# Kernel optimization log

Measured on AMD Instinct MI355X. Metric: run time of the kernel, lower is better.

## Reference

```python
import jax, jax.numpy as jnp
import numpy as np

MUL = 16          # env_embed_multiplicity
LAT = 128         # latent dim
NUM_LAYERS = 2
AVG_N = 20.0      # avg_num_neighbors -> env_sum_normalizations = rsqrt(avg_n)
P = 6.0           # PolynomialCutoff_p


def _mlp(x, w1, w2):
    # ScalarMLPFunction: Linear -> SiLU -> Linear
    return jax.nn.silu(x @ w1) @ w2


def _poly_cutoff(u, p=P):
    f = (1.0 - ((p + 1.0) * (p + 2.0) / 2.0) * u ** p
         + p * (p + 2.0) * u ** (p + 1.0)
         - (p * (p + 1.0) / 2.0) * u ** (p + 2.0))
    return jnp.where(u < 1.0, f, 0.0)


def _weighter(attr, w):
    # MakeWeightedChannels: attr [E,4] = 1x0e + 1x1o, w [E, MUL*2] (one weight per irrep per channel)
    w = w.reshape(-1, MUL, 2)
    fs = w[:, :, 0] * attr[:, 0:1]                    # [E,MUL] scalar channel
    fv = w[:, :, 1][:, :, None] * attr[:, None, 1:4]  # [E,MUL,3] vector channel
    return fs, fv


def _forward(edge_attr, node_attrs, edge_embed, edge_u,
             w2b1, w2b2, lat1_w1, lat1_w2, env0_w1, env0_w2, env1_w1, env1_w2,
             l2w0_w1, l2w0_w2, l2w1_w1, l2w1_w2, envlin_ws, envlin_wv,
             fl2w_w1, fl2w_w2, edge_index):
    E = edge_attr.shape[0]
    N = node_attrs.shape[0]
    center, neigh = edge_index[0], edge_index[1]
    cut = _poly_cutoff(edge_u)[:, None]               # per-layer cutoffs all = r_max
    norm = np.float32(1.0 / np.sqrt(AVG_N))
    inv_s3 = np.float32(1.0 / np.sqrt(3.0))           # CG norm for 1x1->0
    inv_s2 = np.float32(1.0 / np.sqrt(2.0))           # CG norm for 1x1->1 (cross)
    inv_sm = np.float32(1.0 / np.sqrt(MUL))

    # two-body latent: cat(center types, neighbor types, radial embedding)
    x2b = jnp.concatenate([node_attrs[center], node_attrs[neigh], edge_embed], axis=-1)
    lat = cut * _mlp(x2b, w2b1, w2b2)                 # [E,LAT]
    w0 = _mlp(lat, env0_w1, env0_w2)                  # [E,4*MUL] = edge-embed + env weights
    w_edge, w_env = w0[:, :2 * MUL], w0[:, 2 * MUL:]
    fs, fv = _weighter(edge_attr, w_edge)             # initial edge features (embed_initial_edge)

    latent_in = None
    for l in range(NUM_LAYERS):
        if l > 0:
            # latent resnet (update param = 0 -> sigmoid(0))
            new_lat = cut * _mlp(latent_in, lat1_w1, lat1_w2)
            a = np.float32(jax.nn.sigmoid(0.0))
            c_old = np.float32(1.0 / np.sqrt(a * a + 1.0))
            lat = c_old * lat + (a * c_old) * new_lat
            w_env = _mlp(lat, env1_w1, env1_w2)
        # weighted environment embedding: scatter-sum over neighbors, normalize
        es_e, ev_e = _weighter(edge_attr, w_env)
        env_s = jax.ops.segment_sum(es_e, center, num_segments=N) * norm   # [N,MUL]
        env_v = jax.ops.segment_sum(ev_e, center, num_segments=N) * norm   # [N,MUL,3]
        # env_linear (per-irrep channel mixing)
        env_s = (env_s @ envlin_ws[l]) * inv_sm
        env_v = jnp.einsum('nui,uv->nvi', env_v, envlin_wv[l]) * inv_sm
        es, ev = env_s[center], env_v[center]          # gather back to edges
        # channelwise ('uuu') tensor product, lmax=1: 2 scalar + 3 vector paths
        s1 = fs * es
        s2 = jnp.sum(fv * ev, axis=-1) * inv_s3
        v1 = fs[:, :, None] * ev
        v2 = fv * es[:, :, None]
        v3 = jnp.cross(fv, ev) * inv_s2
        scalars = jnp.stack([s1, s2], axis=-1).reshape(E, 2 * MUL)
        latent_in = jnp.concatenate([lat, scalars], axis=-1)      # [E, LAT+2*MUL]
        # per-edge generated linear (shared_weights=False)
        lw1, lw2 = (l2w0_w1, l2w0_w2) if l == 0 else (l2w1_w1, l2w1_w2)
        lw = _mlp(latent_in, lw1, lw2)                 # [E, 5*MUL*MUL]
        ws = lw[:, :2 * MUL * MUL].reshape(E, 2, MUL, MUL)
        wv = lw[:, 2 * MUL * MUL:].reshape(E, 3, MUL, MUL)
        S = jnp.stack([s1, s2], axis=1)                # [E,2,MUL]
        V = jnp.stack([v1, v2, v3], axis=1)            # [E,3,MUL,3]
        fs = jnp.einsum('epu,epuv->ev', S, ws) * np.float32(1.0 / np.sqrt(2.0 * MUL))
        fv = jnp.einsum('epui,epuv->evi', V, wv) * np.float32(1.0 / np.sqrt(3.0 * MUL))
    # final per-edge linear -> 1x1o output per edge
    fw = _mlp(latent_in, fl2w_w1, fl2w_w2)             # [E,MUL]
    return jnp.einsum('eu,eui->ei', fw, fv) * inv_sm   # [E,3]


def setup_inputs():
    key = jax.random.key(0)
    ks = jax.random.split(key, 24)
    E, N, T, B = 120000, 5000, 4, 8
    def w(k, i, o):
        return jax.random.normal(k, (i, o), jnp.float32) / np.float32(np.sqrt(i))
    return {
        'edge_attr': jax.random.normal(ks[0], (E, 4), jnp.float32),
        'node_attrs': jax.random.uniform(ks[1], (N, T), jnp.float32),
        'edge_embed': jax.random.uniform(ks[2], (E, B), jnp.float32),
        'edge_u': jax.random.uniform(ks[3], (E,), jnp.float32),
        'edge_index': jax.random.randint(ks[4], (2, E), 0, N, jnp.int32),
        'w2b1': w(ks[5], 2 * T + B, LAT), 'w2b2': w(ks[6], LAT, LAT),
        'lat1_w1': w(ks[7], LAT + 2 * MUL, LAT), 'lat1_w2': w(ks[8], LAT, LAT),
        'env0_w1': w(ks[9], LAT, LAT), 'env0_w2': w(ks[10], LAT, 4 * MUL),
        'env1_w1': w(ks[11], LAT, LAT), 'env1_w2': w(ks[12], LAT, 2 * MUL),
        'l2w0_w1': w(ks[13], LAT + 2 * MUL, LAT), 'l2w0_w2': w(ks[14], LAT, 5 * MUL * MUL),
        'l2w1_w1': w(ks[15], LAT + 2 * MUL, LAT), 'l2w1_w2': w(ks[16], LAT, 5 * MUL * MUL),
        'envlin_ws': jax.random.normal(ks[17], (NUM_LAYERS, MUL, MUL), jnp.float32),
        'envlin_wv': jax.random.normal(ks[18], (NUM_LAYERS, MUL, MUL), jnp.float32),
        'fl2w_w1': w(ks[19], LAT + 2 * MUL, LAT), 'fl2w_w2': w(ks[20], LAT, MUL),
    }


def reference(edge_attr, node_attrs, edge_embed, edge_u, edge_index,
              w2b1, w2b2, lat1_w1, lat1_w2, env0_w1, env0_w2, env1_w1, env1_w2,
              l2w0_w1, l2w0_w2, l2w1_w1, l2w1_w2, envlin_ws, envlin_wv,
              fl2w_w1, fl2w_w2):
    return _forward(edge_attr, node_attrs, edge_embed, edge_u,
                    w2b1, w2b2, lat1_w1, lat1_w2, env0_w1, env0_w2, env1_w1, env1_w2,
                    l2w0_w1, l2w0_w2, l2w1_w1, l2w1_w2, envlin_ws, envlin_wv,
                    fl2w_w1, fl2w_w2, edge_index)
```

## Files before the change

kernel.cpp:

```cpp
#include <hip/hip_runtime.h>

typedef _Float16 half_t;
typedef _Float16 half8 __attribute__((ext_vector_type(8)));
typedef _Float16 half2_t __attribute__((ext_vector_type(2)));
typedef float f32x16 __attribute__((ext_vector_type(16)));
typedef float f32x4 __attribute__((ext_vector_type(4)));

#define DEVINL __device__ __forceinline__

#define INV_S3 0.57735026918962576f
#define INV_S2 0.70710678118654752f
#define C_OLD  0.89442719099991588f
#define A_COLD 0.44721359549995794f
#define SC_ENV 0.05590169943749474f
#define SC_FS  0.17677669529663688f
#define SC_FV  0.14433756729740643f
#define SC_OUT 0.03608439182435161f
#define SSD 34
#define VPH 146

DEVINL float silu_f(float x) { return x / (1.f + __expf(-x)); }

DEVINL float poly_cut(float u) {
    float u2 = u * u, u4 = u2 * u2, u6 = u4 * u2;
    float f = 1.f - 28.f * u6 + 48.f * u6 * u - 21.f * u6 * u2;
    return (u < 1.f) ? f : 0.f;
}

DEVINL float pkh(float a, float b) {
    half2_t h; h[0] = (half_t)a; h[1] = (half_t)b;
    return __builtin_bit_cast(float, h);
}
DEVINL float2 uph(float p) {
    half2_t h = __builtin_bit_cast(half2_t, p);
    return make_float2((float)h[0], (float)h[1]);
}
DEVINL half8 mk8(const float* w) {
    f32x4 v = {w[0], w[1], w[2], w[3]};
    return __builtin_bit_cast(half8, v);
}
DEVINL float ld_pk2(const half_t* p) {
    half2_t h; h[0] = p[0]; h[1] = p[1];
    return __builtin_bit_cast(float, h);
}
DEVINL float ntl_f(const float* p) { return __builtin_nontemporal_load(p); }
DEVINL f32x4 ntl_f4(const void* p) {
    return __builtin_nontemporal_load((const f32x4*)p);
}
DEVINL f32x4 ld_f4(const void* p) { return *reinterpret_cast<const f32x4*>(p); }
DEVINL void st_h8(half8 v, half_t* p) { *reinterpret_cast<half8*>(p) = v; }
DEVINL void st_f4(const f32x4& v, float* p) { *reinterpret_cast<f32x4*>(p) = v; }

template <int KB>
DEVINL f32x16 colstage(const half_t* __restrict__ Wg, const float* B, int mtile,
                       int nl, int q) {
    const half_t* ap = Wg + (((size_t)mtile * KB + q) * 32 + nl) * 8;
    constexpr int H = KB / 2;
    f32x16 acc0;
#pragma unroll
    for (int i = 0; i < 16; ++i) acc0[i] = 0.f;
    if constexpr (H < 2) {
        half8 a = *reinterpret_cast<const half8*>(ap);
        acc0 = __builtin_amdgcn_mfma_f32_32x32x16_f16(a, mk8(B), acc0, 0, 0, 0);
        return acc0;
    } else {
        f32x16 acc1;
#pragma unroll
        for (int i = 0; i < 16; ++i) acc1[i] = 0.f;
#pragma unroll
        for (int h = 0; h + 1 < H; h += 2) {
            half8 a0 = *reinterpret_cast<const half8*>(ap + h * 512);
            half8 a1 = *reinterpret_cast<const half8*>(ap + (h + 1) * 512);
            acc0 = __builtin_amdgcn_mfma_f32_32x32x16_f16(a0, mk8(B + h * 4), acc0, 0, 0, 0);
            acc1 = __builtin_amdgcn_mfma_f32_32x32x16_f16(a1, mk8(B + (h + 1) * 4), acc1, 0, 0, 0);
        }
        if constexpr (H & 1) {
            half8 a = *reinterpret_cast<const half8*>(ap + (H - 1) * 512);
            acc0 = __builtin_amdgcn_mfma_f32_32x32x16_f16(a, mk8(B + (H - 1) * 4), acc0, 0, 0, 0);
        }
        return acc0 + acc1;
    }
}

template <int KB>
DEVINL f32x16 colstage_lds(const half_t* W, const float* B, int nl, int q) {
    const half_t* ap = W + (q * 32 + nl) * 8;
    constexpr int H = KB / 2;
    f32x16 acc0, acc1;
#pragma unroll
    for (int i = 0; i < 16; ++i) { acc0[i] = 0.f; acc1[i] = 0.f; }
#pragma unroll
    for (int h = 0; h + 1 < H; h += 2) {
        half8 a0 = *reinterpret_cast<const half8*>(ap + h * 512);
        half8 a1 = *reinterpret_cast<const half8*>(ap + (h + 1) * 512);
        acc0 = __builtin_amdgcn_mfma_f32_32x32x16_f16(a0, mk8(B + h * 4), acc0, 0, 0, 0);
        acc1 = __builtin_amdgcn_mfma_f32_32x32x16_f16(a1, mk8(B + (h + 1) * 4), acc1, 0, 0, 0);
    }
    if constexpr (H & 1) {
        half8 a = *reinterpret_cast<const half8*>(ap + (H - 1) * 512);
        acc0 = __builtin_amdgcn_mfma_f32_32x32x16_f16(a, mk8(B + (H - 1) * 4), acc0, 0, 0, 0);
    }
    return acc0 + acc1;
}

struct WFrag { half8 a[8]; };

DEVINL f32x16 mfma8w(const WFrag& f, const float* B) {
    f32x16 acc0, acc1;
#pragma unroll
    for (int i = 0; i < 16; ++i) { acc0[i] = 0.f; acc1[i] = 0.f; }
#pragma unroll
    for (int h = 0; h < 8; h += 2) {
        acc0 = __builtin_amdgcn_mfma_f32_32x32x16_f16(f.a[h], mk8(B + h * 4), acc0, 0, 0, 0);
        acc1 = __builtin_amdgcn_mfma_f32_32x32x16_f16(f.a[h + 1], mk8(B + (h + 1) * 4), acc1, 0, 0, 0);
    }
    return acc0 + acc1;
}

DEVINL void silu16(f32x16& a) {
#pragma unroll
    for (int i = 0; i < 16; ++i) a[i] = silu_f(a[i]);
}

DEVINL void d2b(const f32x16& d, int lane, int q, float* wA, float* wB) {
    float pk[8];
#pragma unroll
    for (int a2 = 0; a2 < 4; ++a2) {
        pk[a2 * 2 + 0] = pkh(d[4 * a2 + 0], d[4 * a2 + 1]);
        pk[a2 * 2 + 1] = pkh(d[4 * a2 + 2], d[4 * a2 + 3]);
    }
#pragma unroll
    for (int t = 0; t < 2; ++t) {
        float k0 = q ? pk[(2 * t + 1) * 2 + 0] : pk[(2 * t) * 2 + 0];
        float k1 = q ? pk[(2 * t + 1) * 2 + 1] : pk[(2 * t) * 2 + 1];
        float s0 = q ? pk[(2 * t) * 2 + 0] : pk[(2 * t + 1) * 2 + 0];
        float s1 = q ? pk[(2 * t) * 2 + 1] : pk[(2 * t + 1) * 2 + 1];
        float r0 = __shfl(s0, lane ^ 32, 64);
        float r1 = __shfl(s1, lane ^ 32, 64);
        float* w = t ? wB : wA;
        w[0] = q ? r0 : k0;
        w[1] = q ? r1 : k1;
        w[2] = q ? k0 : r0;
        w[3] = q ? k1 : r1;
    }
}

DEVINL void ld5(const f32x4* src, f32x4* st, int tid) {
#pragma unroll
    for (int k = 0; k < 5; ++k) st[k] = ld_f4(src + k * 128 + tid);
}
DEVINL void ld4(const f32x4* src, f32x4* st, int tid) {
#pragma unroll
    for (int k = 0; k < 4; ++k) st[k] = ld_f4(src + k * 128 + tid);
}
DEVINL void wr5(f32x4* dst, const f32x4* st, int tid) {
#pragma unroll
    for (int k = 0; k < 5; ++k) dst[k * 128 + tid] = st[k];
}
DEVINL void wr4(f32x4* dst, const f32x4* st, int tid) {
#pragma unroll
    for (int k = 0; k < 4; ++k) dst[k * 128 + tid] = st[k];
}

__global__ __launch_bounds__(256) void k_zero(float* __restrict__ p, int n) {
    int i = blockIdx.x * 256 + threadIdx.x;
    if (i < n) p[i] = 0.f;
}

struct PackArgs {
    const float* src[14];
    half_t* dst[14];
    int K[14];
    int N[14];
};

__global__ __launch_bounds__(256) void k_pack(PackArgs pa) {
    int mi = blockIdx.y;
    int K = pa.K[mi], N = pa.N[mi];
    int Npad = (N + 31) & ~31;
    int KB = K >> 3;
    int cells = KB * Npad;
    int cell = blockIdx.x * 256 + threadIdx.x;
    if (cell >= cells) return;
    int nn = cell & 31, r2 = cell >> 5;
    int kblk = r2 % KB, ntile = r2 / KB;
    int n = ntile * 32 + nn;
    const float* W = pa.src[mi];
    half8 v;
#pragma unroll
    for (int j = 0; j < 8; ++j) {
        int k = kblk * 8 + j;
        v[j] = (half_t)((n < N) ? W[k * N + n] : 0.f);
    }
    *reinterpret_cast<half8*>(pa.dst[mi] + (size_t)cell * 8) = v;
}

__global__ __launch_bounds__(256) void k_hist(const int* __restrict__ eidx,
                                              int* __restrict__ cnt, int E) {
    int e = blockIdx.x * 256 + threadIdx.x;
    if (e < E) atomicAdd(&cnt[eidx[e]], 1);
}

__global__ __launch_bounds__(1024) void k_scan(const int* __restrict__ cnt,
                                               int* __restrict__ start,
                                               int* __restrict__ cursor, int Nn) {
    __shared__ int sh[1024];
    const int t = threadIdx.x;
    const int C = 5;
    int base = t * C;
    int local[C];
    int s = 0;
#pragma unroll
    for (int j = 0; j < C; ++j) {
        int idx = base + j;
        int v = (idx < Nn) ? cnt[idx] : 0;
        local[j] = v;
        s += v;
    }
    sh[t] = s;
    __syncthreads();
    for (int off = 1; off < 1024; off <<= 1) {
        int v = (t >= off) ? sh[t - off] : 0;
        __syncthreads();
        sh[t] += v;
        __syncthreads();
    }
    int run = sh[t] - s;
#pragma unroll
    for (int j = 0; j < C; ++j) {
        int idx = base + j;
        if (idx < Nn) {
            start[idx] = run;
            cursor[idx] = run;
            run += local[j];
        }
    }
    if (t == 1023) start[Nn] = sh[1023];
}

__global__ __launch_bounds__(256) void k_bucket(const int* __restrict__ eidx,
                                                int* __restrict__ cursor,
                                                int* __restrict__ eord, int E) {
    int e = blockIdx.x * 256 + threadIdx.x;
    if (e < E) {
        int pos = atomicAdd(&cursor[eidx[e]], 1);
        eord[pos] = e;
    }
}

__global__ __launch_bounds__(128, 4) void k_edge_front(
    const float* __restrict__ g_ea, const float* __restrict__ g_na,
    const float* __restrict__ g_emb, const float* __restrict__ g_eu,
    const int* __restrict__ g_eidx,
    const half_t* __restrict__ b_w2b1, const half_t* __restrict__ b_w2b2,
    const half_t* __restrict__ b_e0w1, const half_t* __restrict__ b_e0w2,
    half_t* __restrict__ g_lat0, float* __restrict__ g_fs, float* __restrict__ g_fv,
    float* __restrict__ contrib, int E) {
    const int lane = threadIdx.x & 63, nl = lane & 31, q = lane >> 5;
    const int g = blockIdx.x * 2 + (threadIdx.x >> 6);
    const int e = g * 32 + nl;
    int ce = g_eidx[e];
    (void)ce;
    float4 ea = *reinterpret_cast<const float4*>(g_ea + e * 4);
    float cut = poly_cut(g_eu[e]);

    float xw[4];
    if (q == 0) {
        int ce0 = g_eidx[e];
        int ne = g_eidx[E + e];
        float4 nc = *reinterpret_cast<const float4*>(g_na + ce0 * 4);
        float4 nn = *reinterpret_cast<const float4*>(g_na + ne * 4);
        xw[0] = pkh(nc.x, nc.y); xw[1] = pkh(nc.z, nc.w);
        xw[2] = pkh(nn.x, nn.y); xw[3] = pkh(nn.z, nn.w);
    } else {
        f32x4 m0 = ntl_f4(g_emb + e * 8);
        f32x4 m1 = ntl_f4(g_emb + e * 8 + 4);
        xw[0] = pkh(m0[0], m0[1]); xw[1] = pkh(m0[2], m0[3]);
        xw[2] = pkh(m1[0], m1[1]); xw[3] = pkh(m1[2], m1[3]);
    }

    float hB[32], lB[32];
#pragma unroll
    for (int c = 0; c < 4; ++c) {
        f32x16 d = colstage<2>(b_w2b1, xw, c, nl, q);
        silu16(d);
        d2b(d, lane, q, &hB[8 * c], &hB[8 * c + 4]);
    }
    half_t* gl = g_lat0 + (size_t)g * 4096;
#pragma unroll
    for (int c = 0; c < 4; ++c) {
        f32x16 d = colstage<16>(b_w2b2, hB, c, nl, q);
#pragma unroll
        for (int i = 0; i < 16; ++i) d[i] *= cut;
        d2b(d, lane, q, &lB[8 * c], &lB[8 * c + 4]);
        st_h8(mk8(&lB[8 * c]), gl + ((4 * c + q) * 32 + nl) * 8);
        st_h8(mk8(&lB[8 * c + 4]), gl + ((4 * c + 2 + q) * 32 + nl) * 8);
    }
#pragma unroll
    for (int c = 0; c < 4; ++c) {
        f32x16 d = colstage<16>(b_e0w1, lB, c, nl, q);
        silu16(d);
        d2b(d, lane, q, &hB[8 * c], &hB[8 * c + 4]);
    }
    {
        f32x16 d0 = colstage<16>(b_e0w2, hB, 0, nl, q);
        f32x16 d1 = colstage<16>(b_e0w2, hB, 1, nl, q);
        float* cp = contrib + (size_t)e * 64;
#pragma unroll
        for (int r = 0; r < 16; ++r) {
            int f = (r & 3) + 8 * (r >> 2) + 4 * q;
            int u = f >> 1;
            float v0 = d0[r], v1 = d1[r];
            if ((f & 1) == 0) {
                g_fs[e * 16 + u] = v0 * ea.x;
                cp[u] = v1 * ea.x;
            } else {
                g_fv[e * 48 + u * 3 + 0] = v0 * ea.y;
                g_fv[e * 48 + u * 3 + 1] = v0 * ea.z;
                g_fv[e * 48 + u * 3 + 2] = v0 * ea.w;
                cp[16 + u * 3 + 0] = v1 * ea.y;
                cp[16 + u * 3 + 1] = v1 * ea.z;
                cp[16 + u * 3 + 2] = v1 * ea.w;
            }
        }
    }
}

__global__ __launch_bounds__(256) void k_node_agg(
    const int* __restrict__ start, const int* __restrict__ eord,
    const float* __restrict__ contrib, const float* __restrict__ wls,
    const float* __restrict__ wlv, float* __restrict__ ls,
    float* __restrict__ lv, int Nn) {
    __shared__ float rawsh[4][64];
    const int t = threadIdx.x & 63;
    const int sub = threadIdx.x >> 6;
    const int n = blockIdx.x * 4 + sub;
    float acc = 0.f;
    if (n < Nn) {
        int s = start[n], en = start[n + 1];
        for (int base = s; base < en; base += 64) {
            int m = en - base; if (m > 64) m = 64;
            int myord = (base + t < en) ? eord[base + t] : 0;
            for (int i = 0; i < m; ++i) {
                int e2 = __shfl(myord, i, 64);
                acc += contrib[(size_t)e2 * 64 + t];
            }
        }
    }
    rawsh[sub][t] = acc;
    __syncthreads();
    if (n < Nn) {
        const float* raws = rawsh[sub];
        if (t < 16) {
            float as = 0.f;
#pragma unroll
            for (int u = 0; u < 16; ++u) as = fmaf(raws[u], wls[u * 16 + t], as);
            ls[n * 16 + t] = as * SC_ENV;
        } else {
            int idx = t - 16;
            int v = idx / 3, c = idx - 3 * v;
            float a = 0.f;
#pragma unroll
            for (int u = 0; u < 16; ++u)
                a = fmaf(raws[16 + u * 3 + c], wlv[u * 16 + v], a);
            lv[n * 48 + v * 3 + c] = a * SC_ENV;
        }
    }
}

__global__ __launch_bounds__(128, 2) void k_foldlat(
    const float* __restrict__ g_ea, const float* __restrict__ g_eu,
    const int* __restrict__ g_eidx,
    const float* __restrict__ g_fs, const float* __restrict__ g_fv,
    float* __restrict__ gfs2, float* __restrict__ gfv2,
    const float* __restrict__ ls0, const float* __restrict__ lv0,
    const half_t* __restrict__ b_lat1w1, const half_t* __restrict__ b_lat1w2,
    const half_t* __restrict__ b_e1w1, const half_t* __restrict__ b_e1w2,
    const half_t* __restrict__ b_gw1, const half_t* __restrict__ b_gw2,
    const half_t* __restrict__ g_lat0, half_t* __restrict__ g_lat1,
    float* __restrict__ contrib, int nblk2, int E) {
    __shared__ __align__(16) char smem[39424];
    const int tid = threadIdx.x;
    const int lane = tid & 63, nl = lane & 31, q = lane >> 5;
    const int wid = tid >> 6;
    const int bid = blockIdx.x;

    if (bid < nblk2) {
        half_t* sS = reinterpret_cast<half_t*>(smem) + wid * (32 * SSD);
        half_t* Vsh = reinterpret_cast<half_t*>(smem + 4352) + wid * (32 * VPH);
        f32x4* Wb0 = reinterpret_cast<f32x4*>(smem + 23040);
        f32x4* Wb1 = Wb0 + 512;
        const int g = bid * 2 + wid;
        const int e = g * 32 + nl;
        int ce = g_eidx[e];

        const f32x4* gsrc = reinterpret_cast<const f32x4*>(b_gw2);
        f32x4 st[4];
#pragma unroll
        for (int k = 0; k < 4; ++k) st[k] = ld_f4(gsrc + k * 128 + tid);

#pragma unroll
        for (int mm = 0; mm < 8; ++mm) {
            int m = q * 8 + mm;
            float fs = ntl_f(g_fs + e * 16 + m);
            float fv0 = ntl_f(g_fv + e * 48 + m * 3 + 0);
            float fv1 = ntl_f(g_fv + e * 48 + m * 3 + 1);
            float fv2 = ntl_f(g_fv + e * 48 + m * 3 + 2);
            float es = ls0[ce * 16 + m];
            float ev0 = lv0[ce * 48 + m * 3 + 0];
            float ev1 = lv0[ce * 48 + m * 3 + 1];
            float ev2 = lv0[ce * 48 + m * 3 + 2];
            sS[nl * SSD + 2 * m + 0] = (half_t)(fs * es);
            sS[nl * SSD + 2 * m + 1] =
                (half_t)((fv0 * ev0 + fv1 * ev1 + fv2 * ev2) * INV_S3);
            half_t* vp = Vsh + nl * VPH;
            vp[m * 3 + 0] = (half_t)(fs * ev0);
            vp[m * 3 + 1] = (half_t)(fs * ev1);
            vp[m * 3 + 2] = (half_t)(fs * ev2);
            vp[(16 + m) * 3 + 0] = (half_t)(fv0 * es);
            vp[(16 + m) * 3 + 1] = (half_t)(fv1 * es);
            vp[(16 + m) * 3 + 2] = (half_t)(fv2 * es);
            vp[(32 + m) * 3 + 0] = (half_t)((fv1 * ev2 - fv2 * ev1) * INV_S2);
            vp[(32 + m) * 3 + 1] = (half_t)((fv2 * ev0 - fv0 * ev2) * INV_S2);
            vp[(32 + m) * 3 + 2] = (half_t)((fv0 * ev1 - fv1 * ev0) * INV_S2);
        }

        float lB[40];
        const half_t* gl0 = g_lat0 + (size_t)g * 4096;
#pragma unroll
        for (int h = 0; h < 8; ++h) {
            f32x4 v = ntl_f4(gl0 + ((2 * h + q) * 32 + nl) * 8);
            lB[h * 4 + 0] = v[0]; lB[h * 4 + 1] = v[1];
            lB[h * 4 + 2] = v[2]; lB[h * 4 + 3] = v[3];
        }
        __syncthreads();

#pragma unroll
        for (int j2 = 0; j2 < 4; ++j2) {
            lB[32 + j2] = ld_pk2(sS + nl * SSD + 8 * q + 2 * j2);
            lB[36 + j2] = ld_pk2(sS + nl * SSD + 16 + 8 * q + 2 * j2);
        }

        float hB[32];
#pragma unroll
        for (int c = 0; c < 4; ++c) {
            f32x16 d = colstage<20>(b_gw1, lB, c, nl, q);
            silu16(d);
            d2b(d, lane, q, &hB[8 * c], &hB[8 * c + 4]);
        }

#pragma unroll
        for (int k = 0; k < 4; ++k) Wb0[k * 128 + tid] = st[k];
        __syncthreads();

        float fsacc[8];
        float fvacc[8][3];
#pragma unroll
        for (int s = 0; s < 8; ++s) {
            fsacc[s] = 0.f;
            fvacc[s][0] = fvacc[s][1] = fvacc[s][2] = 0.f;
        }

        for (int c = 0; c < 40; ++c) {
            const int buf = c & 1;
            f32x4* cur = buf ? Wb1 : Wb0;
            f32x4* nxt = buf ? Wb0 : Wb1;
            if (c + 1 < 40) {
#pragma unroll
                for (int k = 0; k < 4; ++k)
                    st[k] = ld_f4(gsrc + (size_t)(c + 1) * 512 + k * 128 + tid);
            }
            f32x16 d;
            {
                WFrag f;
                const half_t* wp = reinterpret_cast<const half_t*>(cur);
#pragma unroll
                for (int h = 0; h < 8; ++h)
                    f.a[h] = *reinterpret_cast<const half8*>(
                        wp + ((q + 2 * h) * 32 + nl) * 8);
                d = mfma8w(f, hB);
            }
            if (c < 16) {
                int pu0 = 2 * c, pu1 = pu0 + 1;
                float S0 = (float)sS[nl * SSD + 2 * (pu0 & 15) + (pu0 >> 4)];
                float S1 = (float)sS[nl * SSD + 2 * (pu1 & 15) + (pu1 >> 4)];
#pragma unroll
                for (int r = 0; r < 16; ++r) {
                    int a = r >> 2, bb = r & 3, slot = (a & 1) * 4 + bb;
                    fsacc[slot] = fmaf((a < 2) ? S0 : S1, d[r], fsacc[slot]);
                }
            } else {
                int w0i = 2 * c - 32, w1i = w0i + 1;
                const half_t* vp = Vsh + nl * VPH;
                float V00 = (float)vp[w0i * 3], V01 = (float)vp[w0i * 3 + 1], V02 = (float)vp[w0i * 3 + 2];
                float V10 = (float)vp[w1i * 3], V11 = (float)vp[w1i * 3 + 1], V12 = (float)vp[w1i * 3 + 2];
#pragma unroll
                for (int r = 0; r < 16; ++r) {
                    int a = r >> 2, bb = r & 3, slot = (a & 1) * 4 + bb;
                    float x0 = (a < 2) ? V00 : V10;
                    float x1 = (a < 2) ? V01 : V11;
                    float x2 = (a < 2) ? V02 : V12;
                    fvacc[slot][0] = fmaf(x0, d[r], fvacc[slot][0]);
                    fvacc[slot][1] = fmaf(x1, d[r], fvacc[slot][1]);
                    fvacc[slot][2] = fmaf(x2, d[r], fvacc[slot][2]);
                }
            }
            __builtin_amdgcn_sched_barrier(0);
            if (c + 1 < 40) {
#pragma unroll
                for (int k = 0; k < 4; ++k) nxt[k * 128 + tid] = st[k];
            }
            __syncthreads();
        }

        {
            float* fp = gfs2 + e * 16 + 4 * q;
            f32x4 flo = {fsacc[0] * SC_FS, fsacc[1] * SC_FS,
                         fsacc[2] * SC_FS, fsacc[3] * SC_FS};
            f32x4 fhi = {fsacc[4] * SC_FS, fsacc[5] * SC_FS,
                         fsacc[6] * SC_FS, fsacc[7] * SC_FS};
            st_f4(flo, fp);
            st_f4(fhi, fp + 8);
            float t2[24];
#pragma unroll
            for (int s = 0; s < 4; ++s) {
#pragma unroll
                for (int c3 = 0; c3 < 3; ++c3) {
                    t2[s * 3 + c3] = fvacc[s][c3] * SC_FV;
                    t2[12 + s * 3 + c3] = fvacc[4 + s][c3] * SC_FV;
                }
            }
            float* vlo = gfv2 + e * 48 + 12 * q;
            float* vhi = gfv2 + e * 48 + 24 + 12 * q;
#pragma unroll
            for (int i = 0; i < 3; ++i) {
                f32x4 a = {t2[4 * i + 0], t2[4 * i + 1], t2[4 * i + 2], t2[4 * i + 3]};
                f32x4 b = {t2[12 + 4 * i + 0], t2[12 + 4 * i + 1],
                           t2[12 + 4 * i + 2], t2[12 + 4 * i + 3]};
                st_f4(a, vlo + 4 * i);
                st_f4(b, vhi + 4 * i);
            }
        }
    } else {
        half_t* sS = reinterpret_cast<half_t*>(smem) + wid * (32 * SSD);
        f32x4* Wb0 = reinterpret_cast<f32x4*>(smem + 4352);
        f32x4* Wb1 = Wb0 + 640;
        const int b = bid - nblk2;
        const int g = b * 2 + wid;
        const int e = g * 32 + nl;
        int ce = g_eidx[e];

        const f32x4* w11 = reinterpret_cast<const f32x4*>(b_lat1w1);
        const f32x4* w12 = reinterpret_cast<const f32x4*>(b_lat1w2);
        const f32x4* w21 = reinterpret_cast<const f32x4*>(b_e1w1);
        const f32x4* w22 = reinterpret_cast<const f32x4*>(b_e1w2);

        f32x4 st[5];
        ld5(w11, st, tid);

#pragma unroll
        for (int mm = 0; mm < 8; ++mm) {
            int m = q * 8 + mm;
            float fs = ntl_f(g_fs + e * 16 + m);
            float fv0 = ntl_f(g_fv + e * 48 + m * 3 + 0);
            float fv1 = ntl_f(g_fv + e * 48 + m * 3 + 1);
            float fv2 = ntl_f(g_fv + e * 48 + m * 3 + 2);
            float es = ls0[ce * 16 + m];
            float ev0 = lv0[ce * 48 + m * 3 + 0];
            float ev1 = lv0[ce * 48 + m * 3 + 1];
            float ev2 = lv0[ce * 48 + m * 3 + 2];
            sS[nl * SSD + 2 * m + 0] = (half_t)(fs * es);
            sS[nl * SSD + 2 * m + 1] =
                (half_t)((fv0 * ev0 + fv1 * ev1 + fv2 * ev2) * INV_S3);
        }

        float lB[40];
        const half_t* gl0 = g_lat0 + (size_t)g * 4096;
#pragma unroll
        for (int h = 0; h < 8; ++h) {
            f32x4 v = ntl_f4(gl0 + ((2 * h + q) * 32 + nl) * 8);
            lB[h * 4 + 0] = v[0]; lB[h * 4 + 1] = v[1];
            lB[h * 4 + 2] = v[2]; lB[h * 4 + 3] = v[3];
        }
        float4 ea = *reinterpret_cast<const float4*>(g_ea + e * 4);
        float cut = poly_cut(g_eu[e]);

        wr5(Wb0, st, tid);
        __syncthreads();

#pragma unroll
        for (int j2 = 0; j2 < 4; ++j2) {
            lB[32 + j2] = ld_pk2(sS + nl * SSD + 8 * q + 2 * j2);
            lB[36 + j2] = ld_pk2(sS + nl * SSD + 16 + 8 * q + 2 * j2);
        }

        float hB[32];
#pragma unroll
        for (int c = 0; c < 4; ++c) {
            if (c < 3) ld5(w11 + (size_t)(c + 1) * 640, st, tid);
            else       ld4(w12, st, tid);
            f32x16 d = colstage_lds<20>(
                reinterpret_cast<const half_t*>((c & 1) ? Wb1 : Wb0), lB, nl, q);
            silu16(d);
            d2b(d, lane, q, &hB[8 * c], &hB[8 * c + 4]);
            __builtin_amdgcn_sched_barrier(0);
            if (c < 3) wr5(((c + 1) & 1) ? Wb1 : Wb0, st, tid);
            else       wr4(((c + 1) & 1) ? Wb1 : Wb0, st, tid);
            __syncthreads();
        }
        half_t* gl1 = g_lat1 + (size_t)g * 4096;
        float sc = A_COLD * cut;
#pragma unroll
        for (int c = 0; c < 4; ++c) {
            if (c < 3) ld4(w12 + (size_t)(c + 1) * 512, st, tid);
            else       ld4(w21, st, tid);
            f32x16 d = colstage_lds<16>(
                reinterpret_cast<const half_t*>((c & 1) ? Wb1 : Wb0), hB, nl, q);
#pragma unroll
            for (int i = 0; i < 16; ++i) d[i] *= sc;
            float nw[8];
            d2b(d, lane, q, nw, nw + 4);
#pragma unroll
            for (int p = 0; p < 8; ++p) {
                float2 o = uph(lB[8 * c + p]);
                float2 nn2 = uph(nw[p]);
                lB[8 * c + p] = pkh(C_OLD * o.x + nn2.x, C_OLD * o.y + nn2.y);
            }
            st_h8(mk8(&lB[8 * c]), gl1 + ((4 * c + q) * 32 + nl) * 8);
            st_h8(mk8(&lB[8 * c + 4]), gl1 + ((4 * c + 2 + q) * 32 + nl) * 8);
            __builtin_amdgcn_sched_barrier(0);
            wr4(((c + 1) & 1) ? Wb1 : Wb0, st, tid);
            __syncthreads();
        }
#pragma unroll
        for (int c = 0; c < 4; ++c) {
            if (c == 3) ld4(w22, st, tid);
            f32x16 d = colstage_lds<16>(
                reinterpret_cast<const half_t*>((c & 1) ? Wb1 : Wb0), lB, nl, q);
            silu16(d);
            d2b(d, lane, q, &hB[8 * c], &hB[8 * c + 4]);
            if (c < 3) ld4(w21 + (size_t)(c + 1) * 512, st, tid);
            __builtin_amdgcn_sched_barrier(0);
            wr4(((c + 1) & 1) ? Wb1 : Wb0, st, tid);
            __syncthreads();
        }
        {
            f32x16 d = colstage_lds<16>(
                reinterpret_cast<const half_t*>(Wb0), hB, nl, q);
            float* cp = contrib + (size_t)e * 64;
#pragma unroll
            for (int r = 0; r < 16; ++r) {
                int f = (r & 3) + 8 * (r >> 2) + 4 * q;
                int u = f >> 1;
                float val = d[r];
                if ((f & 1) == 0) {
                    cp[u] = val * ea.x;
                } else {
                    cp[16 + u * 3 + 0] = val * ea.y;
                    cp[16 + u * 3 + 1] = val * ea.z;
                    cp[16 + u * 3 + 2] = val * ea.w;
                }
            }
        }
    }
}

__global__ __launch_bounds__(128, 2) void k_layer1(
    const int* __restrict__ g_eidx, const float* __restrict__ gfs2,
    const float* __restrict__ gfv2, const float* __restrict__ ls1,
    const float* __restrict__ lv1,
    const half_t* __restrict__ b_flw1, const half_t* __restrict__ b_flw2,
    const half_t* __restrict__ b_gw1, const half_t* __restrict__ b_gw2,
    const half_t* __restrict__ g_lat1, float* __restrict__ g_out, int E) {
    __shared__ half_t sS2[2][32 * SSD];
    __shared__ half_t Vsh2[2][32 * VPH];
    __shared__ f32x4 Wbuf[2][640];
    const int tid = threadIdx.x;
    const int lane = tid & 63, nl = lane & 31, q = lane >> 5;
    const int wid = tid >> 6;
    const int g = blockIdx.x * 2 + wid;
    const int e = g * 32 + nl;
    int ce = g_eidx[e];
    half_t* sS = sS2[wid];
    half_t* Vsh = Vsh2[wid];

    const f32x4* wf1 = reinterpret_cast<const f32x4*>(b_flw1);
    const f32x4* wf2 = reinterpret_cast<const f32x4*>(b_flw2);
    const f32x4* wg1 = reinterpret_cast<const f32x4*>(b_gw1);
    const f32x4* wg2 = reinterpret_cast<const f32x4*>(b_gw2);

    f32x4 st[5];
    ld5(wf1, st, tid);

#pragma unroll
    for (int mm = 0; mm < 8; ++mm) {
        int m = q * 8 + mm;
        float fs = ntl_f(gfs2 + e * 16 + m);
        float fv0 = ntl_f(gfv2 + e * 48 + m * 3 + 0);
        float fv1 = ntl_f(gfv2 + e * 48 + m * 3 + 1);
        float fv2 = ntl_f(gfv2 + e * 48 + m * 3 + 2);
        float es = ls1[ce * 16 + m];
        float ev0 = lv1[ce * 48 + m * 3 + 0];
        float ev1 = lv1[ce * 48 + m * 3 + 1];
        float ev2 = lv1[ce * 48 + m * 3 + 2];
        sS[nl * SSD + 2 * m + 0] = (half_t)(fs * es);
        sS[nl * SSD + 2 * m + 1] =
            (half_t)((fv0 * ev0 + fv1 * ev1 + fv2 * ev2) * INV_S3);
        half_t* vp = Vsh + nl * VPH;
        vp[m * 3 + 0] = (half_t)(fs * ev0);
        vp[m * 3 + 1] = (half_t)(fs * ev1);
        vp[m * 3 + 2] = (half_t)(fs * ev2);
        vp[(16 + m) * 3 + 0] = (half_t)(fv0 * es);
        vp[(16 + m) * 3 + 1] = (half_t)(fv1 * es);
        vp[(16 + m) * 3 + 2] = (half_t)(fv2 * es);
        vp[(32 + m) * 3 + 0] = (half_t)((fv1 * ev2 - fv2 * ev1) * INV_S2);
        vp[(32 + m) * 3 + 1] = (half_t)((fv2 * ev0 - fv0 * ev2) * INV_S2);
        vp[(32 + m) * 3 + 2] = (half_t)((fv0 * ev1 - fv1 * ev0) * INV_S2);
    }

    float lB[40];
    const half_t* gl1 = g_lat1 + (size_t)g * 4096;
#pragma unroll
    for (int h = 0; h < 8; ++h) {
        f32x4 v = ntl_f4(gl1 + ((2 * h + q) * 32 + nl) * 8);
        lB[h * 4 + 0] = v[0]; lB[h * 4 + 1] = v[1];
        lB[h * 4 + 2] = v[2]; lB[h * 4 + 3] = v[3];
    }

    wr5(&Wbuf[0][0], st, tid);
    __syncthreads();

#pragma unroll
    for (int j2 = 0; j2 < 4; ++j2) {
        lB[32 + j2] = ld_pk2(sS + nl * SSD + 8 * q + 2 * j2);
        lB[36 + j2] = ld_pk2(sS + nl * SSD + 16 + 8 * q + 2 * j2);
    }

    float hB[32];
#pragma unroll
    for (int c = 0; c < 4; ++c) {
        if (c < 3) ld5(wf1 + (size_t)(c + 1) * 640, st, tid);
        else       ld4(wf2, st, tid);
        f32x16 d = colstage_lds<20>(
            reinterpret_cast<const half_t*>(&Wbuf[c & 1][0]), lB, nl, q);
        silu16(d);
        d2b(d, lane, q, &hB[8 * c], &hB[8 * c + 4]);
        __builtin_amdgcn_sched_barrier(0);
        if (c < 3) wr5(&Wbuf[(c + 1) & 1][0], st, tid);
        else       wr4(&Wbuf[(c + 1) & 1][0], st, tid);
        __syncthreads();
    }
    float fw[8];
    {
        ld5(wg1, st, tid);
        f32x16 d = colstage_lds<16>(
            reinterpret_cast<const half_t*>(&Wbuf[0][0]), hB, nl, q);
#pragma unroll
        for (int r = 0; r < 8; ++r) fw[r] = d[r];
        __builtin_amdgcn_sched_barrier(0);
        wr5(&Wbuf[1][0], st, tid);
        __syncthreads();
    }
#pragma unroll
    for (int c = 0; c < 4; ++c) {
        if (c < 3) ld5(wg1 + (size_t)(c + 1) * 640, st, tid);
        else       ld4(wg2 + (size_t)16 * 512, st, tid);
        f32x16 d = colstage_lds<20>(
            reinterpret_cast<const half_t*>(&Wbuf[(c + 1) & 1][0]), lB, nl, q);
        silu16(d);
        d2b(d, lane, q, &hB[8 * c], &hB[8 * c + 4]);
        __builtin_amdgcn_sched_barrier(0);
        if (c < 3) wr5(&Wbuf[c & 1][0], st, tid);
        else       wr4(&Wbuf[c & 1][0], st, tid);
        __syncthreads();
    }
    float fvacc[8][3];
#pragma unroll
    for (int s = 0; s < 8; ++s) fvacc[s][0] = fvacc[s][1] = fvacc[s][2] = 0.f;
    for (int j = 0; j < 24; ++j) {
        const int pb = (j + 1) & 1;
        if (j < 23) {
#pragma unroll
            for (int k = 0; k < 4; ++k)
                st[k] = ld_f4(wg2 + (size_t)(17 + j) * 512 + k * 128 + tid);
        }
        f32x16 d;
        {
            WFrag f;
            const half_t* wp = reinterpret_cast<const half_t*>(&Wbuf[pb][0]);
#pragma unroll
            for (int h = 0; h < 8; ++h)
                f.a[h] = *reinterpret_cast<const half8*>(
                    wp + ((q + 2 * h) * 32 + nl) * 8);
            d = mfma8w(f, hB);
        }
        {
            int w0i = 2 * j, w1i = 2 * j + 1;
            const half_t* vp = Vsh + nl * VPH;
            float V00 = (float)vp[w0i * 3], V01 = (float)vp[w0i * 3 + 1], V02 = (float)vp[w0i * 3 + 2];
            float V10 = (float)vp[w1i * 3], V11 = (float)vp[w1i * 3 + 1], V12 = (float)vp[w1i * 3 + 2];
#pragma unroll
            for (int r = 0; r < 16; ++r) {
                int a = r >> 2, bb = r & 3, slot = (a & 1) * 4 + bb;
                float x0 = (a < 2) ? V00 : V10;
                float x1 = (a < 2) ? V01 : V11;
                float x2 = (a < 2) ? V02 : V12;
                fvacc[slot][0] = fmaf(x0, d[r], fvacc[slot][0]);
                fvacc[slot][1] = fmaf(x1, d[r], fvacc[slot][1]);
                fvacc[slot][2] = fmaf(x2, d[r], fvacc[slot][2]);
            }
        }
        __builtin_amdgcn_sched_barrier(0);
        if (j < 23) wr4(&Wbuf[pb ^ 1][0], st, tid);
        __syncthreads();
    }
    {
        float o0 = 0.f, o1 = 0.f, o2 = 0.f;
#pragma unroll
        for (int s = 0; s < 8; ++s) {
            o0 = fmaf(fw[s], fvacc[s][0], o0);
            o1 = fmaf(fw[s], fvacc[s][1], o1);
            o2 = fmaf(fw[s], fvacc[s][2], o2);
        }
        o0 += __shfl(o0, lane ^ 32, 64);
        o1 += __shfl(o1, lane ^ 32, 64);
        o2 += __shfl(o2, lane ^ 32, 64);
        if (q == 0) {
            g_out[e * 3 + 0] = o0 * SC_OUT;
            g_out[e * 3 + 1] = o1 * SC_OUT;
            g_out[e * 3 + 2] = o2 * SC_OUT;
        }
    }
}

extern "C" void kernel_launch(void* const* d_in, const int* in_sizes, int n_in,
                              void* d_out, int out_size, void* d_ws, size_t ws_size,
                              hipStream_t stream) {
    const float* g_ea = (const float*)d_in[0];
    const float* g_na = (const float*)d_in[1];
    const float* g_emb = (const float*)d_in[2];
    const float* g_eu = (const float*)d_in[3];
    const int* g_eidx = (const int*)d_in[4];
    const float* w2b1 = (const float*)d_in[5];
    const float* w2b2 = (const float*)d_in[6];
    const float* lat1w1 = (const float*)d_in[7];
    const float* lat1w2 = (const float*)d_in[8];
    const float* e0w1 = (const float*)d_in[9];
    const float* e0w2 = (const float*)d_in[10];
    const float* e1w1 = (const float*)d_in[11];
    const float* e1w2 = (const float*)d_in[12];
    const float* l2w0w1 = (const float*)d_in[13];
    const float* l2w0w2 = (const float*)d_in[14];
    const float* l2w1w1 = (const float*)d_in[15];
    const float* l2w1w2 = (const float*)d_in[16];
    const float* envws = (const float*)d_in[17];
    const float* envwv = (const float*)d_in[18];
    const float* flw1 = (const float*)d_in[19];
    const float* flw2 = (const float*)d_in[20];
    float* out = (float*)d_out;

    const int E = in_sizes[3];
    const int Nn = in_sizes[1] / 4;
    const int nblk = E / 32;
    const int nblk2 = nblk / 2;

    float* p = (float*)d_ws;
    float* gfs = p;  p += (size_t)E * 16;
    float* gfv = p;  p += (size_t)E * 48;
    float* gfs2 = p; p += (size_t)E * 16;
    float* gfv2 = p; p += (size_t)E * 48;
    float* contrib = p; p += (size_t)E * 64;
    float* ls0 = p;  p += (size_t)Nn * 16;
    float* lv0 = p;  p += (size_t)Nn * 48;
    float* ls1 = p;  p += (size_t)Nn * 16;
    float* lv1 = p;  p += (size_t)Nn * 48;
    half_t* hp = (half_t*)p;
    half_t* lat0h = hp; hp += (size_t)nblk * 4096;
    half_t* lat1h = hp; hp += (size_t)nblk * 4096;

    const int KN[14][2] = {{16, 128}, {128, 128}, {128, 128}, {128, 64},
                           {160, 128}, {128, 128}, {128, 128}, {128, 32},
                           {160, 128}, {128, 1280}, {160, 128}, {128, 1280},
                           {160, 128}, {128, 16}};
    const float* srcs[14] = {w2b1, w2b2, e0w1, e0w2, lat1w1, lat1w2, e1w1, e1w2,
                             l2w0w1, l2w0w2, l2w1w1, l2w1w2, flw1, flw2};
    PackArgs pa;
    half_t* bptr[14];
    for (int i = 0; i < 14; ++i) {
        int K = KN[i][0], N = KN[i][1];
        int Npad = (N + 31) & ~31;
        bptr[i] = hp;
        hp += (size_t)K * Npad;
        pa.src[i] = srcs[i];
        pa.dst[i] = bptr[i];
        pa.K[i] = K;
        pa.N[i] = N;
    }
    int* ip = (int*)hp;
    int* cnt = ip;    ip += Nn;
    int* cursor = ip; ip += Nn;
    int* startp = ip; ip += Nn + 1;
    int* eord = ip;   ip += E;

    k_pack<<<dim3(80, 14), 256, 0, stream>>>(pa);
    k_zero<<<(Nn + 255) / 256, 256, 0, stream>>>((float*)cnt, Nn);
    k_hist<<<(E + 255) / 256, 256, 0, stream>>>(g_eidx, cnt, E);
    k_scan<<<1, 1024, 0, stream>>>(cnt, startp, cursor, Nn);
    k_bucket<<<(E + 255) / 256, 256, 0, stream>>>(g_eidx, cursor, eord, E);

    k_edge_front<<<nblk2, 128, 0, stream>>>(g_ea, g_na, g_emb, g_eu, g_eidx,
                                            bptr[0], bptr[1], bptr[2], bptr[3],
                                            lat0h, gfs, gfv, contrib, E);
    const int nagg = (Nn + 3) / 4;
    k_node_agg<<<nagg, 256, 0, stream>>>(startp, eord, contrib, envws, envwv,
                                         ls0, lv0, Nn);
    k_foldlat<<<nblk, 128, 0, stream>>>(g_ea, g_eu, g_eidx, gfs, gfv, gfs2, gfv2,
                                        ls0, lv0, bptr[4], bptr[5], bptr[6],
                                        bptr[7], bptr[8], bptr[9], lat0h, lat1h,
                                        contrib, nblk2, E);
    k_node_agg<<<nagg, 256, 0, stream>>>(startp, eord, contrib, envws + 256,
                                         envwv + 256, ls1, lv1, Nn);
    k_layer1<<<nblk2, 128, 0, stream>>>(g_eidx, gfs2, gfv2, ls1, lv1,
                                        bptr[12], bptr[13], bptr[10], bptr[11],
                                        lat1h, out, E);
}
```

Measured before the change: 436.4 us.

## Stage edge-front MLP weights through double-buffered LDS with prefetch

The edge-front kernel now stages each weight column block (w2b2, env0 w1, env0 w2) into a double-buffered shared-memory tile, prefetching the next block into registers while the current matmul stage reads from LDS. The aim is to replace repeated per-wave global weight loads with one cooperative load per block, overlapped with the MFMA work. It adds block-wide barriers and 16 KB of LDS per block, and it lowers the launch-bounds occupancy hint from 4 to 2 blocks.

```diff
diff --git a/kernel.cpp b/kernel.cpp
--- a/kernel.cpp
+++ b/kernel.cpp
@@ -248,7 +248,7 @@
     }
 }
 
-__global__ __launch_bounds__(128, 4) void k_edge_front(
+__global__ __launch_bounds__(128, 2) void k_edge_front(
     const float* __restrict__ g_ea, const float* __restrict__ g_na,
     const float* __restrict__ g_emb, const float* __restrict__ g_eu,
     const int* __restrict__ g_eidx,
@@ -256,13 +256,21 @@
     const half_t* __restrict__ b_e0w1, const half_t* __restrict__ b_e0w2,
     half_t* __restrict__ g_lat0, float* __restrict__ g_fs, float* __restrict__ g_fv,
     float* __restrict__ contrib, int E) {
-    const int lane = threadIdx.x & 63, nl = lane & 31, q = lane >> 5;
-    const int g = blockIdx.x * 2 + (threadIdx.x >> 6);
+    __shared__ f32x4 Wbuf[2][512];
+    const int tid = threadIdx.x;
+    const int lane = tid & 63, nl = lane & 31, q = lane >> 5;
+    const int wid = tid >> 6;
+    const int g = blockIdx.x * 2 + wid;
     const int e = g * 32 + nl;
-    int ce = g_eidx[e];
-    (void)ce;
     float4 ea = *reinterpret_cast<const float4*>(g_ea + e * 4);
     float cut = poly_cut(g_eu[e]);
+
+    const f32x4* s_w2b2 = reinterpret_cast<const f32x4*>(b_w2b2);
+    const f32x4* s_e0w1 = reinterpret_cast<const f32x4*>(b_e0w1);
+    const f32x4* s_e0w2 = reinterpret_cast<const f32x4*>(b_e0w2);
+
+    f32x4 st[4];
+    ld4(s_w2b2, st, tid);
 
     float xw[4];
     if (q == 0) {
@@ -286,25 +294,50 @@
         silu16(d);
         d2b(d, lane, q, &hB[8 * c], &hB[8 * c + 4]);
     }
+
+    wr4(&Wbuf[0][0], st, tid);
+    __syncthreads();
+
     half_t* gl = g_lat0 + (size_t)g * 4096;
 #pragma unroll
     for (int c = 0; c < 4; ++c) {
-        f32x16 d = colstage<16>(b_w2b2, hB, c, nl, q);
+        if (c < 3) ld4(s_w2b2 + (size_t)(c + 1) * 512, st, tid);
+        else       ld4(s_e0w1, st, tid);
+        f32x16 d = colstage_lds<16>(
+            reinterpret_cast<const half_t*>(&Wbuf[c & 1][0]), hB, nl, q);
 #pragma unroll
         for (int i = 0; i < 16; ++i) d[i] *= cut;
         d2b(d, lane, q, &lB[8 * c], &lB[8 * c + 4]);
         st_h8(mk8(&lB[8 * c]), gl + ((4 * c + q) * 32 + nl) * 8);
         st_h8(mk8(&lB[8 * c + 4]), gl + ((4 * c + 2 + q) * 32 + nl) * 8);
+        __builtin_amdgcn_sched_barrier(0);
+        wr4(&Wbuf[(c + 1) & 1][0], st, tid);
+        __syncthreads();
     }
 #pragma unroll
     for (int c = 0; c < 4; ++c) {
-        f32x16 d = colstage<16>(b_e0w1, lB, c, nl, q);
+        if (c < 3) ld4(s_e0w1 + (size_t)(c + 1) * 512, st, tid);
+        else       ld4(s_e0w2, st, tid);
+        f32x16 d = colstage_lds<16>(
+            reinterpret_cast<const half_t*>(&Wbuf[c & 1][0]), lB, nl, q);
         silu16(d);
         d2b(d, lane, q, &hB[8 * c], &hB[8 * c + 4]);
-    }
+        __builtin_amdgcn_sched_barrier(0);
+        wr4(&Wbuf[(c + 1) & 1][0], st, tid);
+        __syncthreads();
+    }
+    f32x16 d0, d1;
     {
-        f32x16 d0 = colstage<16>(b_e0w2, hB, 0, nl, q);
-        f32x16 d1 = colstage<16>(b_e0w2, hB, 1, nl, q);
+        ld4(s_e0w2 + 512, st, tid);
+        d0 = colstage_lds<16>(
+            reinterpret_cast<const half_t*>(&Wbuf[0][0]), hB, nl, q);
+        __builtin_amdgcn_sched_barrier(0);
+        wr4(&Wbuf[1][0], st, tid);
+        __syncthreads();
+        d1 = colstage_lds<16>(
+            reinterpret_cast<const half_t*>(&Wbuf[1][0]), hB, nl, q);
+    }
+    {
         float* cp = contrib + (size_t)e * 64;
 #pragma unroll
         for (int r = 0; r < 16; ++r) {
```

Measured after the change: 430.8 us (median of 2 runs). Within noise of the previous version (-1.3%).
